# Kernel tuning notes

Hardware: AMD Instinct MI355X
Metric: run time of the kernel (lower is better)

## Reference

```python
import jax, jax.numpy as jnp
import numpy as np

DIM = 1024
HEADS = 16
HEAD_DIM = DIM // HEADS  # 64
B, T, S = 4, 2048, 2048
NEG = -1e9


def rotary_pos_emb(x, freqs):
    # x: (B, H, L, Dh), freqs: (L, Dh//2). Rotate interleaved (even, odd) pairs.
    cos = jnp.cos(freqs)[None, None, :, :]  # (1,1,L,Dh//2)
    sin = jnp.sin(freqs)[None, None, :, :]
    x_even = x[..., 0::2]
    x_odd = x[..., 1::2]
    r_even = x_even * cos - x_odd * sin
    r_odd = x_even * sin + x_odd * cos
    return jnp.stack([r_even, r_odd], axis=-1).reshape(x.shape)


def setup_inputs() -> dict:
    key = jax.random.key(0)
    ks = jax.random.split(key, 9)
    w_std = 1.0 / np.sqrt(DIM)
    return {
        "q_x": jax.random.normal(ks[0], (B, T, DIM), jnp.float32),
        "kv_x": jax.random.normal(ks[1], (B, S, DIM), jnp.float32),
        "freq_q": jax.random.normal(ks[2], (T, HEAD_DIM // 2), jnp.float32),
        "freq_kv": jax.random.normal(ks[3], (S, HEAD_DIM // 2), jnp.float32),
        "key_padding_mask": jax.random.randint(ks[4], (B, S), 0, 2, jnp.int32),
        "Wq": jax.random.normal(ks[5], (DIM, DIM), jnp.float32) * w_std,
        "Wk": jax.random.normal(ks[6], (DIM, DIM), jnp.float32) * w_std,
        "Wv": jax.random.normal(ks[7], (DIM, DIM), jnp.float32) * w_std,
        "Wproj": jax.random.normal(ks[8], (DIM, DIM), jnp.float32) * w_std,
    }


def reference(q_x, kv_x, freq_q, freq_kv, key_padding_mask, Wq, Wk, Wv, Wproj):
    b, t, d = q_x.shape
    s = kv_x.shape[1]
    # QKV projections (torch Linear: x @ W.T), split into heads -> (B, H, L, Dh)
    q = (q_x @ Wq.T).reshape(b, t, HEADS, HEAD_DIM).transpose(0, 2, 1, 3)
    k = (kv_x @ Wk.T).reshape(b, s, HEADS, HEAD_DIM).transpose(0, 2, 1, 3)
    v = (kv_x @ Wv.T).reshape(b, s, HEADS, HEAD_DIM).transpose(0, 2, 1, 3)
    # Rotary embedding on q and k
    q = rotary_pos_emb(q, freq_q)
    k = rotary_pos_emb(k, freq_kv)
    # Scaled dot-product attention with key-padding mask (True = attend)
    scale = HEAD_DIM ** (-0.5)
    scores = jnp.einsum('bhtd,bhsd->bhts', q, k) * scale
    mask = key_padding_mask.astype(bool)[:, None, None, :]  # (B,1,1,S)
    scores = jnp.where(mask, scores, NEG)
    attn = jax.nn.softmax(scores, axis=-1)
    out = jnp.einsum('bhts,bhsd->bhtd', attn, v)
    out = out.transpose(0, 2, 1, 3).reshape(b, t, d)
    return out @ Wproj.T
```

## Files before the change

kernel.cpp:

```cpp
#include <hip/hip_runtime.h>
#include <hip/hip_bf16.h>


typedef __bf16 bf16;
typedef __bf16 bf16x8 __attribute__((ext_vector_type(8)));
typedef __bf16 bf16x4 __attribute__((ext_vector_type(4)));
typedef float  f32x4  __attribute__((ext_vector_type(4)));

#define NB   4
#define NT   2048
#define NS   2048
#define NH   16
#define HD   64
#define SCL  0.18033688011112043f

__device__ __forceinline__ void gload16(const void* g, void* l) {
  __builtin_amdgcn_global_load_lds((const __attribute__((address_space(1))) void*)g,
                                   (__attribute__((address_space(3))) void*)l, 16, 0, 0);
}

__device__ __forceinline__ f32x4 mfma16(bf16x8 a, bf16x8 b, f32x4 c) {
  return __builtin_amdgcn_mfma_f32_16x16x32_bf16(a, b, c, 0, 0, 0);
}

__global__ void k_convert(const float* __restrict__ qx, const float* __restrict__ kvx,
                          const float* __restrict__ Wq, const float* __restrict__ Wk,
                          const float* __restrict__ Wv, const float* __restrict__ Wp,
                          bf16* __restrict__ wbf, bf16* __restrict__ qxbf,
                          bf16* __restrict__ kvxbf)
{
  const long total = 4194304L + 8388608L + 8388608L;
  for (long v = (long)blockIdx.x * blockDim.x + threadIdx.x; v * 4 < total;
       v += (long)gridDim.x * blockDim.x) {
    long e0 = v * 4;
    const float* src; bf16* dst;
    if (e0 < 4194304L) {
      int widx = (int)(e0 >> 20);
      const float* wsrc = (widx == 0) ? Wq : (widx == 1) ? Wk : (widx == 2) ? Wv : Wp;
      src = wsrc + (e0 & 1048575); dst = wbf + e0;
    } else if (e0 < 12582912L) {
      src = qx + (e0 - 4194304L); dst = qxbf + (e0 - 4194304L);
    } else {
      src = kvx + (e0 - 12582912L); dst = kvxbf + (e0 - 12582912L);
    }
    float4 f = *(const float4*)src;
    bf16x4 o = {(bf16)f.x, (bf16)f.y, (bf16)f.z, (bf16)f.w};
    *(bf16x4*)dst = o;
  }
}

__global__ void k_tables(const float* __restrict__ fq, const float* __restrict__ fkv,
                         const int* __restrict__ mask,
                         float2* __restrict__ csq, float2* __restrict__ cskv,
                         float* __restrict__ bias)
{
  int i = blockIdx.x * blockDim.x + threadIdx.x;
  if (i < 65536) {
    float s, c; sincosf(fq[i], &s, &c); csq[i] = make_float2(c, s);
  } else if (i < 131072) {
    int j = i - 65536;
    float s, c; sincosf(fkv[j], &s, &c); cskv[j] = make_float2(c, s);
  } else if (i < 139264) {
    int j = i - 131072;
    bias[j] = mask[j] ? 0.0f : -1.0e9f;
  }
}

template<int EPI>
__global__ __launch_bounds__(256) void k_gemm(
    const bf16* __restrict__ A0, const bf16* __restrict__ A1,
    const bf16* __restrict__ wbase,
    bf16* __restrict__ Qb, bf16* __restrict__ Kb, bf16* __restrict__ Vtb,
    float* __restrict__ Of,
    const float2* __restrict__ csq, const float2* __restrict__ cskv)
{
  __shared__ bf16 As[128 * 32];
  __shared__ bf16 Bs[128 * 32];
  const int z  = (EPI == 0) ? blockIdx.z : 0;
  const bf16* A = (EPI == 1) ? A0 : ((z == 0) ? A0 : A1);
  const bf16* W = wbase + (size_t)z * 1048576;
  const int m0 = blockIdx.x * 128, n0 = blockIdx.y * 128;
  const int tid = threadIdx.x, lane = tid & 63, w = tid >> 6;
  const int g = lane >> 4, c = lane & 15;
  const int wr = w >> 1, wc = w & 1;

  f32x4 acc[4][4];
#pragma unroll
  for (int i = 0; i < 4; ++i)
#pragma unroll
    for (int j = 0; j < 4; ++j) acc[i][j] = 0.0f;

  const bf16* gA = A + (size_t)(m0 + w * 32 + (lane >> 2)) * 1024 + (lane & 3) * 8;
  const bf16* gB = W + (size_t)(n0 + w * 32 + (lane >> 2)) * 1024 + (lane & 3) * 8;
  bf16* lA = As + w * 1024;
  bf16* lB = Bs + w * 1024;

  for (int k0 = 0; k0 < 1024; k0 += 32) {
    __syncthreads();
    gload16(gA, lA);               gload16(gA + 16 * 1024, lA + 512);
    gload16(gB, lB);               gload16(gB + 16 * 1024, lB + 512);
    gA += 32; gB += 32;
    __syncthreads();

    bf16x8 af[4], bfr[4];
#pragma unroll
    for (int mi = 0; mi < 4; ++mi)
      af[mi] = *(const bf16x8*)(As + (wr * 64 + mi * 16 + c) * 32 + g * 8);
#pragma unroll
    for (int ni = 0; ni < 4; ++ni)
      bfr[ni] = *(const bf16x8*)(Bs + (wc * 64 + ni * 16 + c) * 32 + g * 8);
#pragma unroll
    for (int mi = 0; mi < 4; ++mi)
#pragma unroll
      for (int ni = 0; ni < 4; ++ni)
        acc[mi][ni] = mfma16(af[mi], bfr[ni], acc[mi][ni]);
  }

  if (EPI == 1) {
#pragma unroll
    for (int mi = 0; mi < 4; ++mi)
#pragma unroll
      for (int ni = 0; ni < 4; ++ni)
#pragma unroll
        for (int r = 0; r < 4; ++r) {
          int m = m0 + wr * 64 + mi * 16 + g * 4 + r;
          int n = n0 + wc * 64 + ni * 16 + c;
          Of[(size_t)m * 1024 + n] = acc[mi][ni][r];
        }
  } else if (z < 2) {
    const float2* cs = (z == 0) ? csq : cskv;
    bf16* Out = (z == 0) ? Qb : Kb;
#pragma unroll
    for (int mi = 0; mi < 4; ++mi)
#pragma unroll
      for (int ni = 0; ni < 4; ++ni)
#pragma unroll
        for (int r = 0; r < 4; ++r) {
          int m = m0 + wr * 64 + mi * 16 + g * 4 + r;
          int n = n0 + wc * 64 + ni * 16 + c;
          float v = acc[mi][ni][r];
          float p = __shfl_xor(v, 1);
          int t = m & 2047, b = m >> 11;
          int h = n >> 6, d = n & 63;
          float2 cv = cs[t * 32 + (d >> 1)];
          float rot = (d & 1) ? (v * cv.x + p * cv.y)
                              : (v * cv.x - p * cv.y);
          Out[((size_t)((b * 16 + h) * 2048 + t)) * 64 + d] = (bf16)rot;
        }
  } else {
#pragma unroll
    for (int mi = 0; mi < 4; ++mi)
#pragma unroll
      for (int ni = 0; ni < 4; ++ni) {
        int m = m0 + wr * 64 + mi * 16 + g * 4;
        int n = n0 + wc * 64 + ni * 16 + c;
        int b = m >> 11, sl = m & 2047;
        int h = n >> 6, d = n & 63;
        bf16x4 pk = {(bf16)acc[mi][ni][0], (bf16)acc[mi][ni][1],
                     (bf16)acc[mi][ni][2], (bf16)acc[mi][ni][3]};
        *(bf16x4*)(Vtb + ((size_t)((b * 16 + h) * 64 + d)) * 2048 + sl) = pk;
      }
  }
}

__global__ __launch_bounds__(256) void k_attn(
    const bf16* __restrict__ Qb, const bf16* __restrict__ Kb,
    const bf16* __restrict__ Vtb, const float* __restrict__ bias,
    bf16* __restrict__ Ob)
{
  __shared__ bf16 Ks[64 * 64];
  __shared__ bf16 Vs[64 * 64];
  __shared__ bf16 Ps[4 * 16 * 64];
  const int bh = blockIdx.y, b = bh >> 4, h = bh & 15;
  const int t0 = blockIdx.x * 64;
  const int tid = threadIdx.x, lane = tid & 63, w = tid >> 6;
  const int g = lane >> 4, c = lane & 15;

  bf16x8 qf[2];
  {
    const bf16* qp = Qb + ((size_t)bh * 2048 + t0 + w * 16 + c) * 64;
    qf[0] = *(const bf16x8*)(qp + g * 8);
    qf[1] = *(const bf16x8*)(qp + 32 + g * 8);
  }

  float mrun[4], lrun[4];
  f32x4 o[4];
#pragma unroll
  for (int r = 0; r < 4; ++r) { mrun[r] = -3.0e38f; lrun[r] = 0.0f; }
#pragma unroll
  for (int ni = 0; ni < 4; ++ni) o[ni] = 0.0f;

  const int srow8 = lane >> 3;
  const int scol  = ((lane & 7) ^ srow8) * 8;
  const bf16* gK = Kb  + ((size_t)bh * 2048 + w * 16 + srow8) * 64 + scol;
  const bf16* gV = Vtb + ((size_t)bh * 64 + w * 16 + srow8) * 2048 + scol;
  bf16* lK = Ks + w * 1024;
  bf16* lV = Vs + w * 1024;
  const float* bp = bias + b * 2048;

  for (int s0 = 0; s0 < 2048; s0 += 64) {
    __syncthreads();
    gload16(gK, lK);            gload16(gK + 512,      lK + 512);
    gload16(gV, lV);            gload16(gV + 8 * 2048, lV + 512);
    gK += 64 * 64; gV += 64;
    __syncthreads();

    f32x4 sc[4];
#pragma unroll
    for (int st = 0; st < 4; ++st) sc[st] = 0.0f;
#pragma unroll
    for (int kd = 0; kd < 2; ++kd)
#pragma unroll
      for (int st = 0; st < 4; ++st) {
        int srow = st * 16 + c;
        bf16x8 kf = *(const bf16x8*)(Ks + srow * 64 + ((kd * 4 + g) ^ (srow & 7)) * 8);
        sc[st] = mfma16(qf[kd], kf, sc[st]);
      }

    float sv[4][4];
#pragma unroll
    for (int st = 0; st < 4; ++st) {
      float bc = bp[s0 + st * 16 + c];
#pragma unroll
      for (int r = 0; r < 4; ++r) sv[st][r] = sc[st][r] * SCL + bc;
    }

    float mnew[4], corr[4], rsum[4];
#pragma unroll
    for (int r = 0; r < 4; ++r) {
      float mt = fmaxf(fmaxf(sv[0][r], sv[1][r]), fmaxf(sv[2][r], sv[3][r]));
      mt = fmaxf(mt, __shfl_xor(mt, 1));
      mt = fmaxf(mt, __shfl_xor(mt, 2));
      mt = fmaxf(mt, __shfl_xor(mt, 4));
      mt = fmaxf(mt, __shfl_xor(mt, 8));
      mnew[r] = fmaxf(mrun[r], mt);
      corr[r] = exp2f(mrun[r] - mnew[r]);
      mrun[r] = mnew[r];
      rsum[r] = 0.0f;
    }
    char* pbase = (char*)Ps + w * 2048;
#pragma unroll
    for (int st = 0; st < 4; ++st)
#pragma unroll
      for (int r = 0; r < 4; ++r) {
        float p = exp2f(sv[st][r] - mnew[r]);
        rsum[r] += p;
        int t = g * 4 + r;
        *(bf16*)(pbase + t * 128 + ((st * 32 + c * 2) ^ ((t & 7) << 4))) = (bf16)p;
      }
#pragma unroll
    for (int r = 0; r < 4; ++r) {
      float s = rsum[r];
      s += __shfl_xor(s, 1); s += __shfl_xor(s, 2);
      s += __shfl_xor(s, 4); s += __shfl_xor(s, 8);
      lrun[r] = lrun[r] * corr[r] + s;
    }
#pragma unroll
    for (int ni = 0; ni < 4; ++ni)
#pragma unroll
      for (int r = 0; r < 4; ++r) o[ni][r] *= corr[r];

    asm volatile("s_waitcnt lgkmcnt(0)" ::: "memory");
    __builtin_amdgcn_sched_barrier(0);

#pragma unroll
    for (int ks = 0; ks < 2; ++ks) {
      bf16x8 pf = *(const bf16x8*)(pbase + c * 128 +
                                   ((((ks * 4 + g) << 4) ^ ((c & 7) << 4))));
#pragma unroll
      for (int ni = 0; ni < 4; ++ni) {
        int vrow = ni * 16 + c;
        bf16x8 vf = *(const bf16x8*)(Vs + vrow * 64 + (((ks * 4 + g) ^ (vrow & 7)) * 8));
        o[ni] = mfma16(pf, vf, o[ni]);
      }
    }
  }

#pragma unroll
  for (int r = 0; r < 4; ++r) lrun[r] = 1.0f / lrun[r];
#pragma unroll
  for (int ni = 0; ni < 4; ++ni)
#pragma unroll
    for (int r = 0; r < 4; ++r) {
      int t = t0 + w * 16 + g * 4 + r;
      int d = ni * 16 + c;
      Ob[((size_t)(b * 2048 + t)) * 1024 + h * 64 + d] = (bf16)(o[ni][r] * lrun[r]);
    }
}

extern "C" void kernel_launch(void* const* d_in, const int* in_sizes, int n_in,
                              void* d_out, int out_size, void* d_ws, size_t ws_size,
                              hipStream_t stream)
{
  const float* qx  = (const float*)d_in[0];
  const float* kvx = (const float*)d_in[1];
  const float* fq  = (const float*)d_in[2];
  const float* fkv = (const float*)d_in[3];
  const int*  mask = (const int*)  d_in[4];
  const float* Wq  = (const float*)d_in[5];
  const float* Wk  = (const float*)d_in[6];
  const float* Wv  = (const float*)d_in[7];
  const float* Wp  = (const float*)d_in[8];

  char* ws = (char*)d_ws;
  bf16*   wbf   = (bf16*)(ws);
  bf16*   qxbf  = (bf16*)(ws + 8388608);
  bf16*   kvxbf = (bf16*)(ws + 25165824);
  bf16*   Qb    = (bf16*)(ws + 41943040);
  bf16*   Kb    = (bf16*)(ws + 58720256);
  bf16*   Vtb   = (bf16*)(ws + 75497472);
  bf16*   Ob    = (bf16*)(ws + 92274688);
  float2* csq   = (float2*)(ws + 109051904);
  float2* cskv  = (float2*)(ws + 109576192);
  float*  bias  = (float*)(ws + 110100480);
  float*  out   = (float*)d_out;

  k_convert<<<4096, 256, 0, stream>>>(qx, kvx, Wq, Wk, Wv, Wp, wbf, qxbf, kvxbf);
  k_tables<<<544, 256, 0, stream>>>(fq, fkv, mask, csq, cskv, bias);
  k_gemm<0><<<dim3(64, 8, 3), 256, 0, stream>>>(qxbf, kvxbf, wbf,
                                                Qb, Kb, Vtb, nullptr, csq, cskv);
  k_attn<<<dim3(32, 64), 256, 0, stream>>>(Qb, Kb, Vtb, bias, Ob);
  k_gemm<1><<<dim3(64, 8, 1), 256, 0, stream>>>(Ob, nullptr, wbf + 3 * 1048576,
                                                nullptr, nullptr, nullptr, out, csq, cskv);
}
```

Before: 458.0 us.

## Keep softmax probabilities in registers via transposed MFMA and lazy rescaling

```diff
diff --git a/kernel.cpp b/kernel.cpp
--- a/kernel.cpp
+++ b/kernel.cpp
@@ -156,9 +156,12 @@
         int n = n0 + wc * 64 + ni * 16 + c;
         int b = m >> 11, sl = m & 2047;
         int h = n >> 6, d = n & 63;
+        int p  = sl & 63;
+        int st = p >> 4, q4 = (p >> 2) & 3;
+        int col = (sl & ~63) | ((st >> 1) << 5) | (q4 << 3) | ((st & 1) << 2);
         bf16x4 pk = {(bf16)acc[mi][ni][0], (bf16)acc[mi][ni][1],
                      (bf16)acc[mi][ni][2], (bf16)acc[mi][ni][3]};
-        *(bf16x4*)(Vtb + ((size_t)((b * 16 + h) * 64 + d)) * 2048 + sl) = pk;
+        *(bf16x4*)(Vtb + ((size_t)((b * 16 + h) * 64 + d)) * 2048 + col) = pk;
       }
   }
 }
@@ -169,12 +172,19 @@
     bf16* __restrict__ Ob)
 {
   __shared__ bf16 Ks[64 * 64];
-  __shared__ bf16 Vs[64 * 64];
-  __shared__ bf16 Ps[4 * 16 * 64];
+  __shared__ bf16 Vs[80 * 64];
   const int bh = blockIdx.y, b = bh >> 4, h = bh & 15;
   const int t0 = blockIdx.x * 64;
   const int tid = threadIdx.x, lane = tid & 63, w = tid >> 6;
   const int g = lane >> 4, c = lane & 15;
+
+  {
+    int rr = tid >> 4;
+    int col4 = (tid & 15) * 4;
+    bf16 v = (rr == 0) ? (bf16)1.0f : (bf16)0.0f;
+    bf16x4 vv = {v, v, v, v};
+    *(bf16x4*)(Vs + (64 + rr) * 64 + col4) = vv;
+  }
 
   bf16x8 qf[2];
   {
@@ -183,12 +193,10 @@
     qf[1] = *(const bf16x8*)(qp + 32 + g * 8);
   }
 
-  float mrun[4], lrun[4];
-  f32x4 o[4];
-#pragma unroll
-  for (int r = 0; r < 4; ++r) { mrun[r] = -3.0e38f; lrun[r] = 0.0f; }
-#pragma unroll
-  for (int ni = 0; ni < 4; ++ni) o[ni] = 0.0f;
+  float mrun = -3.0e38f;
+  f32x4 o[5];
+#pragma unroll
+  for (int ni = 0; ni < 5; ++ni) o[ni] = 0.0f;
 
   const int srow8 = lane >> 3;
   const int scol  = ((lane & 7) ^ srow8) * 8;
@@ -196,13 +204,17 @@
   const bf16* gV = Vtb + ((size_t)bh * 64 + w * 16 + srow8) * 2048 + scol;
   bf16* lK = Ks + w * 1024;
   bf16* lV = Vs + w * 1024;
-  const float* bp = bias + b * 2048;
+  const float* bp = bias + b * 2048 + g * 4;
 
   for (int s0 = 0; s0 < 2048; s0 += 64) {
     __syncthreads();
     gload16(gK, lK);            gload16(gK + 512,      lK + 512);
     gload16(gV, lV);            gload16(gV + 8 * 2048, lV + 512);
     gK += 64 * 64; gV += 64;
+    float4 bv0 = *(const float4*)(bp + s0);
+    float4 bv1 = *(const float4*)(bp + s0 + 16);
+    float4 bv2 = *(const float4*)(bp + s0 + 32);
+    float4 bv3 = *(const float4*)(bp + s0 + 48);
     __syncthreads();
 
     f32x4 sc[4];
@@ -214,78 +226,64 @@
       for (int st = 0; st < 4; ++st) {
         int srow = st * 16 + c;
         bf16x8 kf = *(const bf16x8*)(Ks + srow * 64 + ((kd * 4 + g) ^ (srow & 7)) * 8);
-        sc[st] = mfma16(qf[kd], kf, sc[st]);
+        sc[st] = mfma16(kf, qf[kd], sc[st]);
       }
 
     float sv[4][4];
 #pragma unroll
-    for (int st = 0; st < 4; ++st) {
-      float bc = bp[s0 + st * 16 + c];
-#pragma unroll
-      for (int r = 0; r < 4; ++r) sv[st][r] = sc[st][r] * SCL + bc;
+    for (int r = 0; r < 4; ++r) {
+      sv[0][r] = sc[0][r] * SCL + ((const float*)&bv0)[r];
+      sv[1][r] = sc[1][r] * SCL + ((const float*)&bv1)[r];
+      sv[2][r] = sc[2][r] * SCL + ((const float*)&bv2)[r];
+      sv[3][r] = sc[3][r] * SCL + ((const float*)&bv3)[r];
     }
 
-    float mnew[4], corr[4], rsum[4];
-#pragma unroll
-    for (int r = 0; r < 4; ++r) {
-      float mt = fmaxf(fmaxf(sv[0][r], sv[1][r]), fmaxf(sv[2][r], sv[3][r]));
-      mt = fmaxf(mt, __shfl_xor(mt, 1));
-      mt = fmaxf(mt, __shfl_xor(mt, 2));
-      mt = fmaxf(mt, __shfl_xor(mt, 4));
-      mt = fmaxf(mt, __shfl_xor(mt, 8));
-      mnew[r] = fmaxf(mrun[r], mt);
-      corr[r] = exp2f(mrun[r] - mnew[r]);
-      mrun[r] = mnew[r];
-      rsum[r] = 0.0f;
+    float mt = sv[0][0];
+#pragma unroll
+    for (int st = 0; st < 4; ++st)
+#pragma unroll
+      for (int r = 0; r < 4; ++r) mt = fmaxf(mt, sv[st][r]);
+    mt = fmaxf(mt, __shfl_xor(mt, 16));
+    mt = fmaxf(mt, __shfl_xor(mt, 32));
+
+    if (__any(mt > mrun + 8.0f)) {
+      float mnew = fmaxf(mrun, mt);
+      float corr = exp2f(mrun - mnew);
+      mrun = mnew;
+#pragma unroll
+      for (int ni = 0; ni < 5; ++ni) o[ni] *= corr;
     }
-    char* pbase = (char*)Ps + w * 2048;
-#pragma unroll
-    for (int st = 0; st < 4; ++st)
-#pragma unroll
-      for (int r = 0; r < 4; ++r) {
-        float p = exp2f(sv[st][r] - mnew[r]);
-        rsum[r] += p;
-        int t = g * 4 + r;
-        *(bf16*)(pbase + t * 128 + ((st * 32 + c * 2) ^ ((t & 7) << 4))) = (bf16)p;
+
+    bf16x8 pf[2];
+#pragma unroll
+    for (int ks = 0; ks < 2; ++ks)
+#pragma unroll
+      for (int st2 = 0; st2 < 2; ++st2) {
+        int st = ks * 2 + st2;
+#pragma unroll
+        for (int r = 0; r < 4; ++r)
+          pf[ks][st2 * 4 + r] = (bf16)exp2f(sv[st][r] - mrun);
       }
-#pragma unroll
-    for (int r = 0; r < 4; ++r) {
-      float s = rsum[r];
-      s += __shfl_xor(s, 1); s += __shfl_xor(s, 2);
-      s += __shfl_xor(s, 4); s += __shfl_xor(s, 8);
-      lrun[r] = lrun[r] * corr[r] + s;
-    }
-#pragma unroll
-    for (int ni = 0; ni < 4; ++ni)
-#pragma unroll
-      for (int r = 0; r < 4; ++r) o[ni][r] *= corr[r];
-
-    asm volatile("s_waitcnt lgkmcnt(0)" ::: "memory");
-    __builtin_amdgcn_sched_barrier(0);
-
-#pragma unroll
-    for (int ks = 0; ks < 2; ++ks) {
-      bf16x8 pf = *(const bf16x8*)(pbase + c * 128 +
-                                   ((((ks * 4 + g) << 4) ^ ((c & 7) << 4))));
-#pragma unroll
-      for (int ni = 0; ni < 4; ++ni) {
+
+#pragma unroll
+    for (int ks = 0; ks < 2; ++ks)
+#pragma unroll
+      for (int ni = 0; ni < 5; ++ni) {
         int vrow = ni * 16 + c;
         bf16x8 vf = *(const bf16x8*)(Vs + vrow * 64 + (((ks * 4 + g) ^ (vrow & 7)) * 8));
-        o[ni] = mfma16(pf, vf, o[ni]);
+        o[ni] = mfma16(vf, pf[ks], o[ni]);
       }
-    }
-  }
-
-#pragma unroll
-  for (int r = 0; r < 4; ++r) lrun[r] = 1.0f / lrun[r];
-#pragma unroll
-  for (int ni = 0; ni < 4; ++ni)
-#pragma unroll
-    for (int r = 0; r < 4; ++r) {
-      int t = t0 + w * 16 + g * 4 + r;
-      int d = ni * 16 + c;
-      Ob[((size_t)(b * 2048 + t)) * 1024 + h * 64 + d] = (bf16)(o[ni][r] * lrun[r]);
-    }
+  }
+
+  float l = __shfl(o[4][0], c);
+  float rl = 1.0f / l;
+  int t = t0 + w * 16 + c;
+#pragma unroll
+  for (int ni = 0; ni < 4; ++ni) {
+    bf16x4 ov = {(bf16)(o[ni][0] * rl), (bf16)(o[ni][1] * rl),
+                 (bf16)(o[ni][2] * rl), (bf16)(o[ni][3] * rl)};
+    *(bf16x4*)(Ob + ((size_t)(b * 2048 + t)) * 1024 + h * 64 + ni * 16 + g * 4) = ov;
+  }
 }
 
 extern "C" void kernel_launch(void* const* d_in, const int* in_sizes, int n_in,
```

Result: faster. 374.6 us (-18.2%).
